# Performance work log

Measured on AMD Instinct MI355X. Metric: run time of the kernel, lower is better.

Reference implementation:

```python
import jax, jax.numpy as jnp
import numpy as np

N_HEAD = 16    # config.n_head
T_STEPS = 3    # config.T: PC energy-minimization steps
LR = 0.01      # config.local_learning_rate


def _causal_attention(x, Wq, Wk, Wv):
    # x: [B, S, E] latent activity; generative model f(x) = causal MHA(x)
    B, S, E = x.shape
    D = E // N_HEAD
    def split(h):  # [B,S,E] -> [B,H,S,D]
        return h.reshape(B, S, N_HEAD, D).transpose(0, 2, 1, 3)
    q = split(x @ Wq.T)
    k = split(x @ Wk.T)
    v = split(x @ Wv.T)
    scores = jnp.einsum('bhqd,bhkd->bhqk', q, k) / jnp.sqrt(jnp.asarray(D, x.dtype))
    mask = jnp.tril(jnp.ones((S, S), dtype=bool))
    scores = jnp.where(mask, scores, jnp.asarray(-1e30, x.dtype))
    att = jax.nn.softmax(scores, axis=-1)
    out = jnp.einsum('bhqk,bhkd->bhqd', att, v)
    return out.transpose(0, 2, 1, 3).reshape(B, S, E)


def _pc_infer(target, f):
    # PCLayer: T steps of gradient descent on E(x) = 0.5 * ||target - f(x)||^2
    # x_init = 'zeros'; returns the inferred latent x (PCLayer.get_x).
    x = jnp.zeros_like(target)
    energy = lambda z: 0.5 * jnp.sum((target - f(z)) ** 2)
    g = jax.grad(energy)
    for _ in range(T_STEPS):  # fixed small T: unrolled
        x = x - LR * g(x)
    return x


def setup_inputs() -> dict:
    key = jax.random.key(0)
    ks = jax.random.split(key, 5)
    B, S, E = 2, 1024, 1024
    fc1_x = jax.random.normal(ks[0], (B, S, E), dtype=jnp.float32)
    init = lambda k: 0.02 * jax.random.normal(k, (E, E), dtype=jnp.float32)
    return {
        'fc1_x': fc1_x,
        'Wq': init(ks[1]),
        'Wk': init(ks[2]),
        'Wv': init(ks[3]),
        'Wo': init(ks[4]),
    }


def reference(fc1_x, Wq, Wk, Wv, Wo):
    # Stage 1 (pc_output): infer pre-output latent att_score s.t. output-proj
    # Wo @ att_score ~ fc1_x  (generative model f1(x) = x @ Wo^T, bias=False).
    att_score = _pc_infer(fc1_x, lambda z: z @ Wo.T)
    # Stage 2 (pc_qkv): infer latent x_qkv s.t. causal MHA(x_qkv) ~ att_score.
    x_qkv = _pc_infer(att_score, lambda z: _causal_attention(z, Wq, Wk, Wv))
    return x_qkv
```

## Files before the change

kernel.cpp:

```cpp
#include <hip/hip_runtime.h>
#include <hip/hip_bf16.h>
#include <math.h>

#define S_LEN 1024
#define E_DIM 1024
#define NH 16
#define HD 64
#define M_ROWS 2048
#define BH_CNT 32

static constexpr float LR_C = 0.01f;
static constexpr float SC_C = 0.125f;
static constexpr float C2_C = 0.125f * 1.44269504f;

typedef unsigned short ushort_t;
typedef __attribute__((ext_vector_type(8))) __bf16 bf16x8;
typedef __attribute__((ext_vector_type(4))) float f32x4;

static __device__ inline ushort_t f2bu(float f) {
  __hip_bfloat16 h = __float2bfloat16(f);
  return *(ushort_t*)&h;
}
static __device__ inline bf16x8 ldg8(const ushort_t* p) { return *(const bf16x8*)p; }

static __device__ inline void async_cp16(const ushort_t* g, __bf16* lds_wave_base) {
  __builtin_amdgcn_global_load_lds((const __attribute__((address_space(1))) void*)g,
                                   (__attribute__((address_space(3))) void*)lds_wave_base,
                                   16, 0, 0);
}

__global__ __launch_bounds__(256) void prep_w(const float* __restrict__ W,
                                              ushort_t* __restrict__ Wb,
                                              ushort_t* __restrict__ WTb) {
  __shared__ float ts[64][65];
  int bx = blockIdx.x * 64, by = blockIdx.y * 64;
  int t = threadIdx.x;
  int rr = t >> 6, cc = t & 63;
  #pragma unroll
  for (int p = 0; p < 16; p++) {
    int r = p * 4 + rr;
    float v = W[(size_t)(by + r) * E_DIM + bx + cc];
    ts[r][cc] = v;
    Wb[(size_t)(by + r) * E_DIM + bx + cc] = f2bu(v);
  }
  __syncthreads();
  #pragma unroll
  for (int p = 0; p < 16; p++) {
    int r = p * 4 + rr;
    WTb[(size_t)(bx + r) * E_DIM + by + cc] = f2bu(ts[cc][r]);
  }
}

__global__ __launch_bounds__(256) void k_cast(const float* __restrict__ in,
                                              ushort_t* __restrict__ out, int n4) {
  int i = blockIdx.x * 256 + threadIdx.x;
  if (i < n4) {
    float4 v = ((const float4*)in)[i];
    ushort_t p[4] = {f2bu(v.x), f2bu(v.y), f2bu(v.z), f2bu(v.w)};
    *(uint2*)(out + (size_t)i * 4) = *(uint2*)p;
  }
}

__global__ __launch_bounds__(256) void k_formN(const float* __restrict__ Mf,
                                               const float* __restrict__ M2f,
                                               ushort_t* __restrict__ Nb) {
  int idx = blockIdx.x * 256 + threadIdx.x;
  int i = idx >> 10, j = idx & 1023;
  float v = -3.f * LR_C * LR_C * Mf[idx] + LR_C * LR_C * LR_C * M2f[idx];
  if (i == j) v += 3.f * LR_C;
  Nb[idx] = f2bu(v);
}

__global__ __launch_bounds__(256) void k_scan1(const float* __restrict__ Xs,
                                               float* __restrict__ Sf,
                                               float* __restrict__ tot) {
  int e = blockIdx.x * 256 + threadIdx.x;
  int b = blockIdx.y;
  int z = blockIdx.z;
  float acc = 0.f;
  for (int i = z * 64 + 63; i >= z * 64; i--) {
    size_t idx = ((size_t)b * S_LEN + i) * E_DIM + e;
    acc = fmaf(Xs[idx], 1.0f / (float)(i + 1), acc);
    Sf[idx] = acc;
  }
  tot[((size_t)b * 16 + z) * E_DIM + e] = acc;
}

__global__ __launch_bounds__(256) void k_scan2(const float* __restrict__ Sf,
                                               const float* __restrict__ tot,
                                               ushort_t* __restrict__ Sb) {
  int e = blockIdx.x * 256 + threadIdx.x;
  int b = blockIdx.y;
  int z = blockIdx.z;
  float off = 0.f;
  for (int c = z + 1; c < 16; c++) off += tot[((size_t)b * 16 + c) * E_DIM + e];
  for (int i = z * 64; i < z * 64 + 64; i++) {
    size_t idx = ((size_t)b * S_LEN + i) * E_DIM + e;
    Sb[idx] = f2bu(Sf[idx] + off);
  }
}

template <int MODE, int NSEG>
__global__ __launch_bounds__(256) void gemm_mf(
    const ushort_t* __restrict__ A0, const ushort_t* __restrict__ A1, const ushort_t* __restrict__ A2,
    const ushort_t* __restrict__ B0, const ushort_t* __restrict__ B1, const ushort_t* __restrict__ B2,
    float* __restrict__ Cf,
    ushort_t* __restrict__ Cb0, ushort_t* __restrict__ Cb1, ushort_t* __restrict__ Cb2,
    ushort_t* __restrict__ Ct0, ushort_t* __restrict__ Ct1, ushort_t* __restrict__ Ct2,
    float alpha) {
  const int K = 1024;
  __shared__ __bf16 As[64][32];
  __shared__ __bf16 Bs[64][32];
  int tid = threadIdx.x;
  int m0 = blockIdx.y * 64, n0 = blockIdx.x * 64;

  const ushort_t* Bsel = B0;
  ushort_t* Cbz = Cb0;
  ushort_t* Ctz = Ct0;
  float tsc = 1.0f;
  if (MODE == 0) {
    int z = blockIdx.z;
    Bsel = (z == 0) ? B0 : (z == 1) ? B1 : B2;
    Cbz = (z == 0) ? Cb0 : (z == 1) ? Cb1 : Cb2;
    Ctz = (z == 0) ? Ct0 : (z == 1) ? Ct1 : Ct2;
    tsc = (z == 2) ? 1.0f : SC_C;
  }

  int lane = tid & 63, wave = tid >> 6;
  int wrow = wave >> 1, wcol = wave & 1;
  int fr = lane & 15, q = lane >> 4;

  int srow = wave * 16 + (lane >> 2);
  int scg = ((lane & 3) + (srow >> 1)) & 3;
  int scol = scg * 8;
  __bf16* ldsA = &As[wave * 16][0];
  __bf16* ldsB = &Bs[wave * 16][0];

  int rA0 = wrow * 32 + fr, rA1 = rA0 + 16;
  int rB0 = wcol * 32 + fr, rB1 = rB0 + 16;
  const bf16x8* pa0 = (const bf16x8*)&As[rA0][((q - (rA0 >> 1)) & 3) * 8];
  const bf16x8* pa1 = (const bf16x8*)&As[rA1][((q - (rA1 >> 1)) & 3) * 8];
  const bf16x8* pb0 = (const bf16x8*)&Bs[rB0][((q - (rB0 >> 1)) & 3) * 8];
  const bf16x8* pb1 = (const bf16x8*)&Bs[rB1][((q - (rB1 >> 1)) & 3) * 8];

  f32x4 acc[2][2] = {};

  #pragma unroll 1
  for (int seg = 0; seg < NSEG; seg++) {
    const ushort_t* Aseg = (seg == 0) ? A0 : (seg == 1) ? A1 : A2;
    const ushort_t* Bseg = (MODE == 0) ? Bsel : ((seg == 0) ? B0 : (seg == 1) ? B1 : B2);
    const ushort_t* ga = Aseg + (size_t)(m0 + srow) * K + scol;
    const ushort_t* gb = Bseg + (size_t)(n0 + srow) * K + scol;
    for (int k0 = 0; k0 < K; k0 += 32) {
      __syncthreads();
      async_cp16(ga + k0, ldsA);
      async_cp16(gb + k0, ldsB);
      __syncthreads();
      bf16x8 a0 = *pa0, a1 = *pa1, b0 = *pb0, b1 = *pb1;
      acc[0][0] = __builtin_amdgcn_mfma_f32_16x16x32_bf16(a0, b0, acc[0][0], 0, 0, 0);
      acc[0][1] = __builtin_amdgcn_mfma_f32_16x16x32_bf16(a0, b1, acc[0][1], 0, 0, 0);
      acc[1][0] = __builtin_amdgcn_mfma_f32_16x16x32_bf16(a1, b0, acc[1][0], 0, 0, 0);
      acc[1][1] = __builtin_amdgcn_mfma_f32_16x16x32_bf16(a1, b1, acc[1][1], 0, 0, 0);
    }
  }

  #pragma unroll
  for (int mi = 0; mi < 2; mi++)
    #pragma unroll
    for (int ni = 0; ni < 2; ni++) {
      int col = n0 + wcol * 32 + ni * 16 + fr;
      int row0 = m0 + wrow * 32 + mi * 16 + q * 4;
      ushort_t pk[4];
      #pragma unroll
      for (int r = 0; r < 4; r++) {
        size_t idx = (size_t)(row0 + r) * E_DIM + col;
        float v = acc[mi][ni][r];
        if (MODE == 0) {
          Cbz[idx] = f2bu(v);
          pk[r] = f2bu(v * tsc);
        } else if (MODE == 2) {
          float nv = Cf[idx] + alpha * v;
          Cf[idx] = nv;
          Cb0[idx] = f2bu(nv);
        } else if (MODE == 3) {
          Cf[idx] = v;
        } else if (MODE == 4) {
          Cf[idx] = v;
          Cb0[idx] = f2bu(v);
        } else if (MODE == 6) {
          float nv = alpha * v;
          Cf[idx] = nv;
          Cb0[idx] = f2bu(nv);
        } else {
          Cb0[idx] = f2bu(v);
        }
      }
      if (MODE == 0) {
        int hh = col >> 6, dd = col & 63;
        int bb = row0 >> 10, ss = row0 & 1023;
        *(uint2*)(Ctz + ((size_t)((bb * NH + hh) * HD + dd)) * S_LEN + ss) = *(uint2*)pk;
      }
    }
}


__global__ __launch_bounds__(256) void fwd_fused(const ushort_t* __restrict__ Qg,
                                                 const ushort_t* __restrict__ Kg,
                                                 const ushort_t* __restrict__ Vt,
                                                 const float* __restrict__ Xs,
                                                 float* __restrict__ mbuf,
                                                 ushort_t* __restrict__ Gb,
                                                 ushort_t* __restrict__ Gt,
                                                 float* __restrict__ Dv) {
  int bh = blockIdx.x, y = blockIdx.y;
  int it = (y < 8) ? (15 - y) : (y - 8);
  int b = bh >> 4, h = bh & 15;
  int tid = threadIdx.x, lane = tid & 63, wv = tid >> 6;
  int fr = lane & 15, q = lane >> 4;
  int i0 = it * 64, band = wv * 16;
  __shared__ ushort_t Kts[64][72];
  __shared__ ushort_t Vts[64][72];
  __shared__ ushort_t Ps[64][72];

  const ushort_t* Qrow = Qg + (size_t)(b * S_LEN + i0 + band + fr) * E_DIM + h * HD;
  bf16x8 aq0 = ldg8(Qrow + q * 8);
  bf16x8 aq1 = ldg8(Qrow + 32 + q * 8);

  float m[4], l[4];
  #pragma unroll
  for (int r = 0; r < 4; r++) { m[r] = -1e30f; l[r] = 0.f; }
  f32x4 oacc[4] = {};

  #pragma unroll 1
  for (int jt = 0; jt <= it; jt++) {
    int j0 = jt * 64;
    __syncthreads();
    #pragma unroll
    for (int t = 0; t < 2; t++) {
      int u = tid + 256 * t;
      int r = u >> 3, c8 = (u & 7) * 8;
      *(uint4*)&Kts[r][c8] = *(const uint4*)(Kg + (size_t)(b * S_LEN + j0 + r) * E_DIM + h * HD + c8);
      *(uint4*)&Vts[r][c8] = *(const uint4*)(Vt + (size_t)(bh * HD + r) * S_LEN + j0 + c8);
    }
    __syncthreads();
    f32x4 sA[4];
    #pragma unroll
    for (int nc = 0; nc < 4; nc++) {
      bf16x8 bk0 = *(const bf16x8*)&Kts[nc * 16 + fr][q * 8];
      bf16x8 bk1 = *(const bf16x8*)&Kts[nc * 16 + fr][32 + q * 8];
      f32x4 z = {};
      z = __builtin_amdgcn_mfma_f32_16x16x32_bf16(aq0, bk0, z, 0, 0, 0);
      sA[nc] = __builtin_amdgcn_mfma_f32_16x16x32_bf16(aq1, bk1, z, 0, 0, 0);
    }
    float sv[4][4];
    #pragma unroll
    for (int nc = 0; nc < 4; nc++)
      #pragma unroll
      for (int r = 0; r < 4; r++) {
        int row = i0 + band + q * 4 + r;
        int col = j0 + nc * 16 + fr;
        sv[nc][r] = (col <= row) ? sA[nc][r] * C2_C : -1e30f;
      }
    #pragma unroll
    for (int r = 0; r < 4; r++) {
      float mx = fmaxf(fmaxf(sv[0][r], sv[1][r]), fmaxf(sv[2][r], sv[3][r]));
      #pragma unroll
      for (int off = 1; off < 16; off <<= 1) mx = fmaxf(mx, __shfl_xor(mx, off, 64));
      float mn = fmaxf(m[r], mx);
      float alpha = exp2f(m[r] - mn);
      float ps = 0.f;
      #pragma unroll
      for (int nc = 0; nc < 4; nc++) {
        float p = exp2f(sv[nc][r] - mn);
        Ps[band + q * 4 + r][nc * 16 + fr] = f2bu(p);
        ps += p;
      }
      #pragma unroll
      for (int off = 1; off < 16; off <<= 1) ps += __shfl_xor(ps, off, 64);
      l[r] = l[r] * alpha + ps;
      m[r] = mn;
      #pragma unroll
      for (int nc = 0; nc < 4; nc++) oacc[nc][r] *= alpha;
    }
    bf16x8 ap0 = *(const bf16x8*)&Ps[band + fr][q * 8];
    bf16x8 ap1 = *(const bf16x8*)&Ps[band + fr][32 + q * 8];
    #pragma unroll
    for (int nc = 0; nc < 4; nc++) {
      bf16x8 bv0 = *(const bf16x8*)&Vts[nc * 16 + fr][q * 8];
      bf16x8 bv1 = *(const bf16x8*)&Vts[nc * 16 + fr][32 + q * 8];
      oacc[nc] = __builtin_amdgcn_mfma_f32_16x16x32_bf16(ap0, bv0, oacc[nc], 0, 0, 0);
      oacc[nc] = __builtin_amdgcn_mfma_f32_16x16x32_bf16(ap1, bv1, oacc[nc], 0, 0, 0);
    }
  }
  float linv[4];
  #pragma unroll
  for (int r = 0; r < 4; r++) linv[r] = 1.0f / l[r];
  float dpart[4] = {};
  #pragma unroll
  for (int nc = 0; nc < 4; nc++) {
    ushort_t pg[4];
    #pragma unroll
    for (int r = 0; r < 4; r++) {
      int row = i0 + band + q * 4 + r;
      size_t gi = (size_t)(b * S_LEN + row) * E_DIM + h * HD + nc * 16 + fr;
      float o = oacc[nc][r] * linv[r];
      float g = o - Xs[gi];
      ushort_t bu = f2bu(g);
      Gb[gi] = bu;
      pg[r] = bu;
      dpart[r] += g * o;
    }
    int d = nc * 16 + fr;
    int s0 = i0 + band + q * 4;
    *(uint2*)(Gt + ((size_t)bh * HD + d) * S_LEN + s0) = *(uint2*)pg;
  }
  #pragma unroll
  for (int r = 0; r < 4; r++) {
    #pragma unroll
    for (int off = 1; off < 16; off <<= 1) dpart[r] += __shfl_xor(dpart[r], off, 64);
  }
  if (fr == 0) {
    #pragma unroll
    for (int r = 0; r < 4; r++) {
      size_t sid = (size_t)bh * S_LEN + i0 + band + q * 4 + r;
      mbuf[sid] = m[r] + log2f(l[r]);
      Dv[sid] = dpart[r];
    }
  }
}

__global__ __launch_bounds__(256) void bwd_fused(const ushort_t* __restrict__ Qg,
                                                 const ushort_t* __restrict__ Kg,
                                                 const ushort_t* __restrict__ Vg,
                                                 const ushort_t* __restrict__ Gg,
                                                 const ushort_t* __restrict__ Qt,
                                                 const ushort_t* __restrict__ Kt,
                                                 const ushort_t* __restrict__ Gt,
                                                 const float* __restrict__ mbuf,
                                                 const float* __restrict__ Dv,
                                                 ushort_t* __restrict__ GQ,
                                                 ushort_t* __restrict__ GK,
                                                 ushort_t* __restrict__ GV) {
  int bh = blockIdx.x, y = blockIdx.y;
  int b = bh >> 4, h = bh & 15;
  int tid = threadIdx.x, lane = tid & 63, wv = tid >> 6;
  int fr = lane & 15, q = lane >> 4;
  int band = wv * 16;
  __shared__ ushort_t smem[6][64][72];

  {
    ushort_t (*Kts)[72] = smem[0];
    ushort_t (*Vts)[72] = smem[1];
    ushort_t (*Ktt)[72] = smem[2];
    ushort_t (*dSs)[72] = smem[3];
    int it = y, i0 = it * 64;

    const ushort_t* Qrow = Qg + (size_t)(b * S_LEN + i0 + band + fr) * E_DIM + h * HD;
    const ushort_t* Grow = Gg + (size_t)(b * S_LEN + i0 + band + fr) * E_DIM + h * HD;
    bf16x8 aq0 = ldg8(Qrow + q * 8), aq1 = ldg8(Qrow + 32 + q * 8);
    bf16x8 ag0 = ldg8(Grow + q * 8), ag1 = ldg8(Grow + 32 + q * 8);

    float mrow[4], Dr[4];
    #pragma unroll
    for (int r = 0; r < 4; r++) {
      size_t sid = (size_t)bh * S_LEN + i0 + band + q * 4 + r;
      mrow[r] = mbuf[sid]; Dr[r] = Dv[sid];
    }
    f32x4 dqacc[4] = {};

    #pragma unroll 1
    for (int jt = 0; jt <= it; jt++) {
      int j0 = jt * 64;
      __syncthreads();
      #pragma unroll
      for (int t = 0; t < 2; t++) {
        int u = tid + 256 * t;
        int r = u >> 3, c8 = (u & 7) * 8;
        *(uint4*)&Kts[r][c8] = *(const uint4*)(Kg + (size_t)(b * S_LEN + j0 + r) * E_DIM + h * HD + c8);
        *(uint4*)&Vts[r][c8] = *(const uint4*)(Vg + (size_t)(b * S_LEN + j0 + r) * E_DIM + h * HD + c8);
        *(uint4*)&Ktt[r][c8] = *(const uint4*)(Kt + (size_t)(bh * HD + r) * S_LEN + j0 + c8);
      }
      __syncthreads();
      f32x4 sA[4], dpA[4];
      #pragma unroll
      for (int nc = 0; nc < 4; nc++) {
        bf16x8 bk0 = *(const bf16x8*)&Kts[nc * 16 + fr][q * 8];
        bf16x8 bk1 = *(const bf16x8*)&Kts[nc * 16 + fr][32 + q * 8];
        bf16x8 bv0 = *(const bf16x8*)&Vts[nc * 16 + fr][q * 8];
        bf16x8 bv1 = *(const bf16x8*)&Vts[nc * 16 + fr][32 + q * 8];
        f32x4 z = {};
        z = __builtin_amdgcn_mfma_f32_16x16x32_bf16(aq0, bk0, z, 0, 0, 0);
        sA[nc] = __builtin_amdgcn_mfma_f32_16x16x32_bf16(aq1, bk1, z, 0, 0, 0);
        f32x4 z2 = {};
        z2 = __builtin_amdgcn_mfma_f32_16x16x32_bf16(ag0, bv0, z2, 0, 0, 0);
        dpA[nc] = __builtin_amdgcn_mfma_f32_16x16x32_bf16(ag1, bv1, z2, 0, 0, 0);
      }
      #pragma unroll
      for (int nc = 0; nc < 4; nc++)
        #pragma unroll
        for (int r = 0; r < 4; r++) {
          int row = i0 + band + q * 4 + r;
          int col = j0 + nc * 16 + fr;
          float ds = 0.f;
          if (col <= row) {
            float P = exp2f(fmaf(sA[nc][r], C2_C, -mrow[r]));
            ds = P * (dpA[nc][r] - Dr[r]);
          }
          dSs[band + q * 4 + r][nc * 16 + fr] = f2bu(ds);
        }
      bf16x8 ad0 = *(const bf16x8*)&dSs[band + fr][q * 8];
      bf16x8 ad1 = *(const bf16x8*)&dSs[band + fr][32 + q * 8];
      #pragma unroll
      for (int nc = 0; nc < 4; nc++) {
        bf16x8 bt0 = *(const bf16x8*)&Ktt[nc * 16 + fr][q * 8];
        bf16x8 bt1 = *(const bf16x8*)&Ktt[nc * 16 + fr][32 + q * 8];
        dqacc[nc] = __builtin_amdgcn_mfma_f32_16x16x32_bf16(ad0, bt0, dqacc[nc], 0, 0, 0);
        dqacc[nc] = __builtin_amdgcn_mfma_f32_16x16x32_bf16(ad1, bt1, dqacc[nc], 0, 0, 0);
      }
    }
    #pragma unroll
    for (int nc = 0; nc < 4; nc++)
      #pragma unroll
      for (int r = 0; r < 4; r++) {
        int row = i0 + band + q * 4 + r;
        size_t gi = (size_t)(b * S_LEN + row) * E_DIM + h * HD + nc * 16 + fr;
        GQ[gi] = f2bu(dqacc[nc][r]);
      }
  }

  {
    ushort_t (*Qs_)[72] = smem[0];
    ushort_t (*Gs_)[72] = smem[1];
    ushort_t (*Qtt)[72] = smem[2];
    ushort_t (*Gtt)[72] = smem[3];
    ushort_t (*PT)[72]  = smem[4];
    ushort_t (*dST)[72] = smem[5];
    int jt = y, j0 = jt * 64;

    const ushort_t* Krow = Kg + (size_t)(b * S_LEN + j0 + band + fr) * E_DIM + h * HD;
    const ushort_t* Vrow = Vg + (size_t)(b * S_LEN + j0 + band + fr) * E_DIM + h * HD;
    bf16x8 ak0 = ldg8(Krow + q * 8), ak1 = ldg8(Krow + 32 + q * 8);
    bf16x8 av0 = ldg8(Vrow + q * 8), av1 = ldg8(Vrow + 32 + q * 8);

    f32x4 dkacc[4] = {}, dvacc[4] = {};

    #pragma unroll 1
    for (int i_t = jt; i_t < 16; i_t++) {
      int i0 = i_t * 64;
      __syncthreads();
      #pragma unroll
      for (int t = 0; t < 2; t++) {
        int u = tid + 256 * t;
        int r = u >> 3, c8 = (u & 7) * 8;
        *(uint4*)&Qs_[r][c8] = *(const uint4*)(Qg + (size_t)(b * S_LEN + i0 + r) * E_DIM + h * HD + c8);
        *(uint4*)&Gs_[r][c8] = *(const uint4*)(Gg + (size_t)(b * S_LEN + i0 + r) * E_DIM + h * HD + c8);
        *(uint4*)&Qtt[r][c8] = *(const uint4*)(Qt + (size_t)(bh * HD + r) * S_LEN + i0 + c8);
        *(uint4*)&Gtt[r][c8] = *(const uint4*)(Gt + (size_t)(bh * HD + r) * S_LEN + i0 + c8);
      }
      __syncthreads();
      float mc[4], Dc[4];
      #pragma unroll
      for (int nc = 0; nc < 4; nc++) {
        size_t sid = (size_t)bh * S_LEN + i0 + nc * 16 + fr;
        mc[nc] = mbuf[sid]; Dc[nc] = Dv[sid];
      }
      f32x4 stA[4], dptA[4];
      #pragma unroll
      for (int nc = 0; nc < 4; nc++) {
        bf16x8 bq0 = *(const bf16x8*)&Qs_[nc * 16 + fr][q * 8];
        bf16x8 bq1 = *(const bf16x8*)&Qs_[nc * 16 + fr][32 + q * 8];
        bf16x8 bg0 = *(const bf16x8*)&Gs_[nc * 16 + fr][q * 8];
        bf16x8 bg1 = *(const bf16x8*)&Gs_[nc * 16 + fr][32 + q * 8];
        f32x4 z = {};
        z = __builtin_amdgcn_mfma_f32_16x16x32_bf16(ak0, bq0, z, 0, 0, 0);
        stA[nc] = __builtin_amdgcn_mfma_f32_16x16x32_bf16(ak1, bq1, z, 0, 0, 0);
        f32x4 z2 = {};
        z2 = __builtin_amdgcn_mfma_f32_16x16x32_bf16(av0, bg0, z2, 0, 0, 0);
        dptA[nc] = __builtin_amdgcn_mfma_f32_16x16x32_bf16(av1, bg1, z2, 0, 0, 0);
      }
      #pragma unroll
      for (int nc = 0; nc < 4; nc++)
        #pragma unroll
        for (int r = 0; r < 4; r++) {
          int jrow = j0 + band + q * 4 + r;
          int icol = i0 + nc * 16 + fr;
          float P = 0.f, ds = 0.f;
          if (icol >= jrow) {
            P = exp2f(fmaf(stA[nc][r], C2_C, -mc[nc]));
            ds = P * (dptA[nc][r] - Dc[nc]);
          }
          PT[band + q * 4 + r][nc * 16 + fr] = f2bu(P);
          dST[band + q * 4 + r][nc * 16 + fr] = f2bu(ds);
        }
      bf16x8 ap0 = *(const bf16x8*)&PT[band + fr][q * 8];
      bf16x8 ap1 = *(const bf16x8*)&PT[band + fr][32 + q * 8];
      bf16x8 ad0 = *(const bf16x8*)&dST[band + fr][q * 8];
      bf16x8 ad1 = *(const bf16x8*)&dST[band + fr][32 + q * 8];
      #pragma unroll
      for (int nc = 0; nc < 4; nc++) {
        bf16x8 bg0 = *(const bf16x8*)&Gtt[nc * 16 + fr][q * 8];
        bf16x8 bg1 = *(const bf16x8*)&Gtt[nc * 16 + fr][32 + q * 8];
        bf16x8 bq0 = *(const bf16x8*)&Qtt[nc * 16 + fr][q * 8];
        bf16x8 bq1 = *(const bf16x8*)&Qtt[nc * 16 + fr][32 + q * 8];
        dvacc[nc] = __builtin_amdgcn_mfma_f32_16x16x32_bf16(ap0, bg0, dvacc[nc], 0, 0, 0);
        dvacc[nc] = __builtin_amdgcn_mfma_f32_16x16x32_bf16(ap1, bg1, dvacc[nc], 0, 0, 0);
        dkacc[nc] = __builtin_amdgcn_mfma_f32_16x16x32_bf16(ad0, bq0, dkacc[nc], 0, 0, 0);
        dkacc[nc] = __builtin_amdgcn_mfma_f32_16x16x32_bf16(ad1, bq1, dkacc[nc], 0, 0, 0);
      }
    }
    #pragma unroll
    for (int nc = 0; nc < 4; nc++)
      #pragma unroll
      for (int r = 0; r < 4; r++) {
        int jrow = j0 + band + q * 4 + r;
        size_t gi = (size_t)(b * S_LEN + jrow) * E_DIM + h * HD + nc * 16 + fr;
        GK[gi] = f2bu(dkacc[nc][r]);
        GV[gi] = f2bu(dvacc[nc][r]);
      }
  }
}

extern "C" void kernel_launch(void* const* d_in, const int* in_sizes, int n_in,
                              void* d_out, int out_size, void* d_ws, size_t ws_size,
                              hipStream_t stream) {
  const float* T1 = (const float*)d_in[0];
  const float* Wq = (const float*)d_in[1];
  const float* Wk = (const float*)d_in[2];
  const float* Wv = (const float*)d_in[3];
  const float* Wo = (const float*)d_in[4];

  const size_t M2 = 2097152;
  const size_t M1 = 1048576;
  float* w = (float*)d_ws;
  float* Xs = w;
  float* mS = Xs + M2;
  float* DvS = mS + 65536;
  ushort_t* u = (ushort_t*)(DvS + 65536);
  ushort_t* W0 = u;          ushort_t* W1 = W0 + M1;  ushort_t* W2 = W1 + M1;
  ushort_t* W3 = W2 + M1;    ushort_t* W4 = W3 + M1;  ushort_t* W5 = W4 + M1;
  ushort_t* Qb = W5 + M1;    ushort_t* Kb = Qb + M2;  ushort_t* Vb = Kb + M2;
  ushort_t* Qt = Vb + M2;    ushort_t* Kt = Qt + M2;  ushort_t* Vt = Kt + M2;
  ushort_t* Gt = Vt + M2;
  ushort_t* Gb = Gt + M2;
  ushort_t* GQb = Gb + M2;   ushort_t* GKb = GQb + M2; ushort_t* GVb = GKb + M2;
  ushort_t* X2b = GVb + M2;
  float* X2 = (float*)d_out;

  float* Mf  = (float*)Qb;
  float* M2f = (float*)Kb;
  ushort_t* Mb  = Gt;
  ushort_t* Nb  = Vb;
  ushort_t* AtB = Qt;
  ushort_t* T1b = Kt;

  float* Sf  = (float*)GQb;
  float* tot = mS;
  ushort_t* Sb = GVb;

  dim3 pgrid(16, 16);
  dim3 sgrid(16, 16);
  dim3 ggrid(16, 32);
  dim3 ggrid3(16, 32, 3);
  dim3 agrid(BH_CNT, 16);

  k_cast<<<(M2 / 4 + 255) / 256, 256, 0, stream>>>(T1, T1b, (int)(M2 / 4));
  prep_w<<<pgrid, 256, 0, stream>>>(Wo, W0, W1);
  gemm_mf<4, 1><<<sgrid, 256, 0, stream>>>(W1, nullptr, nullptr, W1, nullptr, nullptr,
                                           Mf, Mb, nullptr, nullptr,
                                           nullptr, nullptr, nullptr, 0.f);
  gemm_mf<3, 1><<<sgrid, 256, 0, stream>>>(Mb, nullptr, nullptr, Mb, nullptr, nullptr,
                                           M2f, nullptr, nullptr, nullptr,
                                           nullptr, nullptr, nullptr, 0.f);
  k_formN<<<(M1 + 255) / 256, 256, 0, stream>>>(Mf, M2f, Nb);
  gemm_mf<5, 1><<<sgrid, 256, 0, stream>>>(Nb, nullptr, nullptr, W0, nullptr, nullptr,
                                           nullptr, AtB, nullptr, nullptr,
                                           nullptr, nullptr, nullptr, 0.f);
  prep_w<<<pgrid, 256, 0, stream>>>(Wq, W0, W3);
  prep_w<<<pgrid, 256, 0, stream>>>(Wk, W1, W4);
  prep_w<<<pgrid, 256, 0, stream>>>(Wv, W2, W5);
  gemm_mf<3, 1><<<ggrid, 256, 0, stream>>>(T1b, nullptr, nullptr, AtB, nullptr, nullptr,
                                           Xs, nullptr, nullptr, nullptr,
                                           nullptr, nullptr, nullptr, 0.f);

  k_scan1<<<dim3(E_DIM / 256, 2, 16), 256, 0, stream>>>(Xs, Sf, tot);
  k_scan2<<<dim3(E_DIM / 256, 2, 16), 256, 0, stream>>>(Sf, tot, Sb);
  gemm_mf<6, 1><<<ggrid, 256, 0, stream>>>(Sb, nullptr, nullptr, W5, nullptr, nullptr,
                                           X2, X2b, nullptr, nullptr,
                                           nullptr, nullptr, nullptr, LR_C);

  for (int t = 1; t < 3; t++) {
    gemm_mf<0, 1><<<ggrid3, 256, 0, stream>>>(X2b, nullptr, nullptr, W0, W1, W2,
                                              nullptr, Qb, Kb, Vb,
                                              Qt, Kt, Vt, 0.f);
    fwd_fused<<<agrid, 256, 0, stream>>>(Qb, Kb, Vt, Xs, mS, Gb, Gt, DvS);
    bwd_fused<<<agrid, 256, 0, stream>>>(Qb, Kb, Vb, Gb, Qt, Kt, Gt, mS, DvS,
                                         GQb, GKb, GVb);
    gemm_mf<2, 3><<<ggrid, 256, 0, stream>>>(GQb, GKb, GVb, W3, W4, W5,
                                             X2, X2b, nullptr, nullptr,
                                             nullptr, nullptr, nullptr, -LR_C);
  }
}
```

Baseline: 456.3 us.

## Split fused attention backward into separate dQ and dK/dV blocks with less shared memory

The attention backward kernel now runs the dQ pass and the dK/dV pass in separate blocks on a doubled grid, instead of running both sequentially inside one block. Shared memory drops from six 64x72 tiles to three by reusing buffers across phases, with extra barriers, and launch bounds request four blocks per CU. The dQ blocks are launched in reverse tile order so the longest causal rows start first. The cost is more __syncthreads per iteration and a second pass over staged data through the reused buffers.

```diff
diff --git a/kernel.cpp b/kernel.cpp
--- a/kernel.cpp
+++ b/kernel.cpp
@@ -329,31 +329,29 @@
   }
 }
 
-__global__ __launch_bounds__(256) void bwd_fused(const ushort_t* __restrict__ Qg,
-                                                 const ushort_t* __restrict__ Kg,
-                                                 const ushort_t* __restrict__ Vg,
-                                                 const ushort_t* __restrict__ Gg,
-                                                 const ushort_t* __restrict__ Qt,
-                                                 const ushort_t* __restrict__ Kt,
-                                                 const ushort_t* __restrict__ Gt,
-                                                 const float* __restrict__ mbuf,
-                                                 const float* __restrict__ Dv,
-                                                 ushort_t* __restrict__ GQ,
-                                                 ushort_t* __restrict__ GK,
-                                                 ushort_t* __restrict__ GV) {
-  int bh = blockIdx.x, y = blockIdx.y;
+__global__ __launch_bounds__(256, 4) void bwd_split(const ushort_t* __restrict__ Qg,
+                                                    const ushort_t* __restrict__ Kg,
+                                                    const ushort_t* __restrict__ Vg,
+                                                    const ushort_t* __restrict__ Gg,
+                                                    const ushort_t* __restrict__ Qt,
+                                                    const ushort_t* __restrict__ Kt,
+                                                    const ushort_t* __restrict__ Gt,
+                                                    const float* __restrict__ mbuf,
+                                                    const float* __restrict__ Dv,
+                                                    ushort_t* __restrict__ GQ,
+                                                    ushort_t* __restrict__ GK,
+                                                    ushort_t* __restrict__ GV) {
+  int bh = blockIdx.x, yy = blockIdx.y;
   int b = bh >> 4, h = bh & 15;
   int tid = threadIdx.x, lane = tid & 63, wv = tid >> 6;
   int fr = lane & 15, q = lane >> 4;
   int band = wv * 16;
-  __shared__ ushort_t smem[6][64][72];
-
-  {
-    ushort_t (*Kts)[72] = smem[0];
-    ushort_t (*Vts)[72] = smem[1];
-    ushort_t (*Ktt)[72] = smem[2];
-    ushort_t (*dSs)[72] = smem[3];
-    int it = y, i0 = it * 64;
+  __shared__ ushort_t b0[64][72];
+  __shared__ ushort_t b1[64][72];
+  __shared__ ushort_t dsb[64][72];
+
+  if (yy < 16) {
+    int it = 15 - yy, i0 = it * 64;
 
     const ushort_t* Qrow = Qg + (size_t)(b * S_LEN + i0 + band + fr) * E_DIM + h * HD;
     const ushort_t* Grow = Gg + (size_t)(b * S_LEN + i0 + band + fr) * E_DIM + h * HD;
@@ -376,24 +374,30 @@
       for (int t = 0; t < 2; t++) {
         int u = tid + 256 * t;
         int r = u >> 3, c8 = (u & 7) * 8;
-        *(uint4*)&Kts[r][c8] = *(const uint4*)(Kg + (size_t)(b * S_LEN + j0 + r) * E_DIM + h * HD + c8);
-        *(uint4*)&Vts[r][c8] = *(const uint4*)(Vg + (size_t)(b * S_LEN + j0 + r) * E_DIM + h * HD + c8);
-        *(uint4*)&Ktt[r][c8] = *(const uint4*)(Kt + (size_t)(bh * HD + r) * S_LEN + j0 + c8);
+        *(uint4*)&b0[r][c8] = *(const uint4*)(Kg + (size_t)(b * S_LEN + j0 + r) * E_DIM + h * HD + c8);
+        *(uint4*)&b1[r][c8] = *(const uint4*)(Vg + (size_t)(b * S_LEN + j0 + r) * E_DIM + h * HD + c8);
       }
       __syncthreads();
       f32x4 sA[4], dpA[4];
       #pragma unroll
       for (int nc = 0; nc < 4; nc++) {
-        bf16x8 bk0 = *(const bf16x8*)&Kts[nc * 16 + fr][q * 8];
-        bf16x8 bk1 = *(const bf16x8*)&Kts[nc * 16 + fr][32 + q * 8];
-        bf16x8 bv0 = *(const bf16x8*)&Vts[nc * 16 + fr][q * 8];
-        bf16x8 bv1 = *(const bf16x8*)&Vts[nc * 16 + fr][32 + q * 8];
+        bf16x8 bk0 = *(const bf16x8*)&b0[nc * 16 + fr][q * 8];
+        bf16x8 bk1 = *(const bf16x8*)&b0[nc * 16 + fr][32 + q * 8];
+        bf16x8 bv0 = *(const bf16x8*)&b1[nc * 16 + fr][q * 8];
+        bf16x8 bv1 = *(const bf16x8*)&b1[nc * 16 + fr][32 + q * 8];
         f32x4 z = {};
         z = __builtin_amdgcn_mfma_f32_16x16x32_bf16(aq0, bk0, z, 0, 0, 0);
         sA[nc] = __builtin_amdgcn_mfma_f32_16x16x32_bf16(aq1, bk1, z, 0, 0, 0);
         f32x4 z2 = {};
         z2 = __builtin_amdgcn_mfma_f32_16x16x32_bf16(ag0, bv0, z2, 0, 0, 0);
         dpA[nc] = __builtin_amdgcn_mfma_f32_16x16x32_bf16(ag1, bv1, z2, 0, 0, 0);
+      }
+      __syncthreads();
+      #pragma unroll
+      for (int t = 0; t < 2; t++) {
+        int u = tid + 256 * t;
+        int r = u >> 3, c8 = (u & 7) * 8;
+        *(uint4*)&b0[r][c8] = *(const uint4*)(Kt + (size_t)(bh * HD + r) * S_LEN + j0 + c8);
       }
       #pragma unroll
       for (int nc = 0; nc < 4; nc++)
@@ -406,14 +410,15 @@
             float P = exp2f(fmaf(sA[nc][r], C2_C, -mrow[r]));
             ds = P * (dpA[nc][r] - Dr[r]);
           }
-          dSs[band + q * 4 + r][nc * 16 + fr] = f2bu(ds);
+          dsb[band + q * 4 + r][nc * 16 + fr] = f2bu(ds);
         }
-      bf16x8 ad0 = *(const bf16x8*)&dSs[band + fr][q * 8];
-      bf16x8 ad1 = *(const bf16x8*)&dSs[band + fr][32 + q * 8];
+      bf16x8 ad0 = *(const bf16x8*)&dsb[band + fr][q * 8];
+      bf16x8 ad1 = *(const bf16x8*)&dsb[band + fr][32 + q * 8];
+      __syncthreads();
       #pragma unroll
       for (int nc = 0; nc < 4; nc++) {
-        bf16x8 bt0 = *(const bf16x8*)&Ktt[nc * 16 + fr][q * 8];
-        bf16x8 bt1 = *(const bf16x8*)&Ktt[nc * 16 + fr][32 + q * 8];
+        bf16x8 bt0 = *(const bf16x8*)&b0[nc * 16 + fr][q * 8];
+        bf16x8 bt1 = *(const bf16x8*)&b0[nc * 16 + fr][32 + q * 8];
         dqacc[nc] = __builtin_amdgcn_mfma_f32_16x16x32_bf16(ad0, bt0, dqacc[nc], 0, 0, 0);
         dqacc[nc] = __builtin_amdgcn_mfma_f32_16x16x32_bf16(ad1, bt1, dqacc[nc], 0, 0, 0);
       }
@@ -426,16 +431,8 @@
         size_t gi = (size_t)(b * S_LEN + row) * E_DIM + h * HD + nc * 16 + fr;
         GQ[gi] = f2bu(dqacc[nc][r]);
       }
-  }
-
-  {
-    ushort_t (*Qs_)[72] = smem[0];
-    ushort_t (*Gs_)[72] = smem[1];
-    ushort_t (*Qtt)[72] = smem[2];
-    ushort_t (*Gtt)[72] = smem[3];
-    ushort_t (*PT)[72]  = smem[4];
-    ushort_t (*dST)[72] = smem[5];
-    int jt = y, j0 = jt * 64;
+  } else {
+    int jt = yy - 16, j0 = jt * 64;
 
     const ushort_t* Krow = Kg + (size_t)(b * S_LEN + j0 + band + fr) * E_DIM + h * HD;
     const ushort_t* Vrow = Vg + (size_t)(b * S_LEN + j0 + band + fr) * E_DIM + h * HD;
@@ -452,10 +449,8 @@
       for (int t = 0; t < 2; t++) {
         int u = tid + 256 * t;
         int r = u >> 3, c8 = (u & 7) * 8;
-        *(uint4*)&Qs_[r][c8] = *(const uint4*)(Qg + (size_t)(b * S_LEN + i0 + r) * E_DIM + h * HD + c8);
-        *(uint4*)&Gs_[r][c8] = *(const uint4*)(Gg + (size_t)(b * S_LEN + i0 + r) * E_DIM + h * HD + c8);
-        *(uint4*)&Qtt[r][c8] = *(const uint4*)(Qt + (size_t)(bh * HD + r) * S_LEN + i0 + c8);
-        *(uint4*)&Gtt[r][c8] = *(const uint4*)(Gt + (size_t)(bh * HD + r) * S_LEN + i0 + c8);
+        *(uint4*)&b0[r][c8] = *(const uint4*)(Qg + (size_t)(b * S_LEN + i0 + r) * E_DIM + h * HD + c8);
+        *(uint4*)&b1[r][c8] = *(const uint4*)(Gg + (size_t)(b * S_LEN + i0 + r) * E_DIM + h * HD + c8);
       }
       __syncthreads();
       float mc[4], Dc[4];
@@ -467,10 +462,10 @@
       f32x4 stA[4], dptA[4];
       #pragma unroll
       for (int nc = 0; nc < 4; nc++) {
-        bf16x8 bq0 = *(const bf16x8*)&Qs_[nc * 16 + fr][q * 8];
-        bf16x8 bq1 = *(const bf16x8*)&Qs_[nc * 16 + fr][32 + q * 8];
-        bf16x8 bg0 = *(const bf16x8*)&Gs_[nc * 16 + fr][q * 8];
-        bf16x8 bg1 = *(const bf16x8*)&Gs_[nc * 16 + fr][32 + q * 8];
+        bf16x8 bq0 = *(const bf16x8*)&b0[nc * 16 + fr][q * 8];
+        bf16x8 bq1 = *(const bf16x8*)&b0[nc * 16 + fr][32 + q * 8];
+        bf16x8 bg0 = *(const bf16x8*)&b1[nc * 16 + fr][q * 8];
+        bf16x8 bg1 = *(const bf16x8*)&b1[nc * 16 + fr][32 + q * 8];
         f32x4 z = {};
         z = __builtin_amdgcn_mfma_f32_16x16x32_bf16(ak0, bq0, z, 0, 0, 0);
         stA[nc] = __builtin_amdgcn_mfma_f32_16x16x32_bf16(ak1, bq1, z, 0, 0, 0);
@@ -478,6 +473,15 @@
         z2 = __builtin_amdgcn_mfma_f32_16x16x32_bf16(av0, bg0, z2, 0, 0, 0);
         dptA[nc] = __builtin_amdgcn_mfma_f32_16x16x32_bf16(av1, bg1, z2, 0, 0, 0);
       }
+      __syncthreads();
+      #pragma unroll
+      for (int t = 0; t < 2; t++) {
+        int u = tid + 256 * t;
+        int r = u >> 3, c8 = (u & 7) * 8;
+        *(uint4*)&b0[r][c8] = *(const uint4*)(Qt + (size_t)(bh * HD + r) * S_LEN + i0 + c8);
+        *(uint4*)&b1[r][c8] = *(const uint4*)(Gt + (size_t)(bh * HD + r) * S_LEN + i0 + c8);
+      }
+      ushort_t dsp[4][4];
       #pragma unroll
       for (int nc = 0; nc < 4; nc++)
         #pragma unroll
@@ -489,21 +493,30 @@
             P = exp2f(fmaf(stA[nc][r], C2_C, -mc[nc]));
             ds = P * (dptA[nc][r] - Dc[nc]);
           }
-          PT[band + q * 4 + r][nc * 16 + fr] = f2bu(P);
-          dST[band + q * 4 + r][nc * 16 + fr] = f2bu(ds);
+          dsp[nc][r] = f2bu(ds);
+          dsb[band + q * 4 + r][nc * 16 + fr] = f2bu(P);
         }
-      bf16x8 ap0 = *(const bf16x8*)&PT[band + fr][q * 8];
-      bf16x8 ap1 = *(const bf16x8*)&PT[band + fr][32 + q * 8];
-      bf16x8 ad0 = *(const bf16x8*)&dST[band + fr][q * 8];
-      bf16x8 ad1 = *(const bf16x8*)&dST[band + fr][32 + q * 8];
+      bf16x8 ap0 = *(const bf16x8*)&dsb[band + fr][q * 8];
+      bf16x8 ap1 = *(const bf16x8*)&dsb[band + fr][32 + q * 8];
+      __syncthreads();
       #pragma unroll
       for (int nc = 0; nc < 4; nc++) {
-        bf16x8 bg0 = *(const bf16x8*)&Gtt[nc * 16 + fr][q * 8];
-        bf16x8 bg1 = *(const bf16x8*)&Gtt[nc * 16 + fr][32 + q * 8];
-        bf16x8 bq0 = *(const bf16x8*)&Qtt[nc * 16 + fr][q * 8];
-        bf16x8 bq1 = *(const bf16x8*)&Qtt[nc * 16 + fr][32 + q * 8];
+        bf16x8 bg0 = *(const bf16x8*)&b1[nc * 16 + fr][q * 8];
+        bf16x8 bg1 = *(const bf16x8*)&b1[nc * 16 + fr][32 + q * 8];
         dvacc[nc] = __builtin_amdgcn_mfma_f32_16x16x32_bf16(ap0, bg0, dvacc[nc], 0, 0, 0);
         dvacc[nc] = __builtin_amdgcn_mfma_f32_16x16x32_bf16(ap1, bg1, dvacc[nc], 0, 0, 0);
+      }
+      #pragma unroll
+      for (int nc = 0; nc < 4; nc++)
+        #pragma unroll
+        for (int r = 0; r < 4; r++)
+          dsb[band + q * 4 + r][nc * 16 + fr] = dsp[nc][r];
+      bf16x8 ad0 = *(const bf16x8*)&dsb[band + fr][q * 8];
+      bf16x8 ad1 = *(const bf16x8*)&dsb[band + fr][32 + q * 8];
+      #pragma unroll
+      for (int nc = 0; nc < 4; nc++) {
+        bf16x8 bq0 = *(const bf16x8*)&b0[nc * 16 + fr][q * 8];
+        bf16x8 bq1 = *(const bf16x8*)&b0[nc * 16 + fr][32 + q * 8];
         dkacc[nc] = __builtin_amdgcn_mfma_f32_16x16x32_bf16(ad0, bq0, dkacc[nc], 0, 0, 0);
         dkacc[nc] = __builtin_amdgcn_mfma_f32_16x16x32_bf16(ad1, bq1, dkacc[nc], 0, 0, 0);
       }
@@ -562,6 +575,7 @@
   dim3 ggrid(16, 32);
   dim3 ggrid3(16, 32, 3);
   dim3 agrid(BH_CNT, 16);
+  dim3 bgrid(BH_CNT, 32);
 
   k_cast<<<(M2 / 4 + 255) / 256, 256, 0, stream>>>(T1, T1b, (int)(M2 / 4));
   prep_w<<<pgrid, 256, 0, stream>>>(Wo, W0, W1);
@@ -593,7 +607,7 @@
                                               nullptr, Qb, Kb, Vb,
                                               Qt, Kt, Vt, 0.f);
     fwd_fused<<<agrid, 256, 0, stream>>>(Qb, Kb, Vt, Xs, mS, Gb, Gt, DvS);
-    bwd_fused<<<agrid, 256, 0, stream>>>(Qb, Kb, Vb, Gb, Qt, Kt, Gt, mS, DvS,
+    bwd_split<<<bgrid, 256, 0, stream>>>(Qb, Kb, Vb, Gb, Qt, Kt, Gt, mS, DvS,
                                          GQb, GKb, GVb);
     gemm_mf<2, 3><<<ggrid, 256, 0, stream>>>(GQb, GKb, GVb, W3, W4, W5,
                                              X2, X2b, nullptr, nullptr,
```

Result: slower. 490.8 us (+7.5%).
